# Optimization experiments

Hardware: AMD Instinct MI355X
Metric: run time of the kernel (lower is better)

Reference implementation:

```python
import jax, jax.numpy as jnp
import numpy as np

N_SRC = 2_000_000   # coords at feat_depth (fine level)
N_TGT = 1_000_000   # coords at feat_depth-1 (coarse level)
E = 8_000_000       # neighbor edges from get_neighbours
C = 32              # feature channels


def setup_inputs() -> dict:
    key = jax.random.key(0)
    k1, k2, k3, k4 = jax.random.split(key, 4)
    feat = jax.random.normal(k1, (N_SRC, C), dtype=jnp.float32)
    src_ids = jax.random.randint(k2, (E,), 0, N_SRC)
    tgt_ids = jax.random.randint(k3, (E,), 0, N_TGT)
    ntypes = jax.random.randint(k4, (E, 3), -1, 27).astype(jnp.int32)
    return {"feat": feat, "src_ids": src_ids, "tgt_ids": tgt_ids,
            "ntypes": ntypes, "n_tgt": N_TGT}


def reference(feat, src_ids, tgt_ids, ntypes, n_tgt):
    # p_masks = torch.all(ntypes >= 0, dim=1)
    p_mask = jnp.all(ntypes >= 0, axis=1)                  # [E] bool
    # Route masked-out edges to a dummy segment (index n_tgt) instead of
    # boolean-filtering, keeping shapes static for jit.
    seg = jnp.where(p_mask, tgt_ids, n_tgt)                # [E]
    gathered = feat[src_ids]                               # [E, C] irregular gather
    sums = jax.ops.segment_sum(gathered, seg, num_segments=n_tgt + 1)[:n_tgt]
    counts = jax.ops.segment_sum(jnp.ones((seg.shape[0],), feat.dtype), seg,
                                 num_segments=n_tgt + 1)[:n_tgt]
    # scatter_mean: empty segments yield 0 (torch_scatter semantics)
    out = jnp.where(counts[:, None] > 0, sums / jnp.maximum(counts[:, None], 1), 0.0)
    return out  # feat_depth - 1 is a trivial python int, omitted
```

## Files before the change

### kernel.cpp

```cpp
#include <hip/hip_runtime.h>


#define CCH 32
#define BSH 10
#define BKT 1024
#define CAP 8960
#define BIN_TILE 8192
typedef unsigned int u32;
typedef float f32x4 __attribute__((ext_vector_type(4)));
typedef int i32x4 __attribute__((ext_vector_type(4)));

__global__ __launch_bounds__(1024) void bin_fixed_kernel(
    const int* __restrict__ src_ids, const int* __restrict__ tgt_ids,
    const int* __restrict__ ntypes, u32* __restrict__ bcur,
    u32* __restrict__ pairs, int E, int NB) {
  __shared__ unsigned short s_b[BIN_TILE];
  __shared__ u32 s_pw[BIN_TILE];
  __shared__ u32 s_cnt[1024];
  const long long base = (long long)blockIdx.x * BIN_TILE;

  s_cnt[threadIdx.x] = 0;
  __syncthreads();

  for (int k = 0; k < BIN_TILE / 4096; ++k) {
    const int i4 = (threadIdx.x + k * 1024) * 4;
    const long long e4 = base + i4;
    int n_or[4];
    int tg[4], sr[4];
    bool any = false;
    if (e4 + 3 < E) {
      const i32x4 w0 = __builtin_nontemporal_load(
          reinterpret_cast<const i32x4*>(ntypes + 3 * e4));
      const i32x4 w1 = __builtin_nontemporal_load(
          reinterpret_cast<const i32x4*>(ntypes + 3 * e4 + 4));
      const i32x4 w2 = __builtin_nontemporal_load(
          reinterpret_cast<const i32x4*>(ntypes + 3 * e4 + 8));
      const i32x4 t4 = __builtin_nontemporal_load(
          reinterpret_cast<const i32x4*>(tgt_ids + e4));
      const i32x4 s4 = __builtin_nontemporal_load(
          reinterpret_cast<const i32x4*>(src_ids + e4));
      n_or[0] = w0.x | w0.y | w0.z;
      n_or[1] = w0.w | w1.x | w1.y;
      n_or[2] = w1.z | w1.w | w2.x;
      n_or[3] = w2.y | w2.z | w2.w;
      tg[0] = t4.x; tg[1] = t4.y; tg[2] = t4.z; tg[3] = t4.w;
      sr[0] = s4.x; sr[1] = s4.y; sr[2] = s4.z; sr[3] = s4.w;
      any = true;
    } else {
#pragma unroll
      for (int j = 0; j < 4; ++j) {
        const long long e = e4 + j;
        if (e < E) {
          const long long eb = 3LL * e;
          n_or[j] = ntypes[eb] | ntypes[eb + 1] | ntypes[eb + 2];
          tg[j] = tgt_ids[e];
          sr[j] = src_ids[e];
          any = true;
        } else {
          n_or[j] = -1;
        }
      }
    }
#pragma unroll
    for (int j = 0; j < 4; ++j) {
      unsigned short bb = 0xFFFFu;
      u32 pw = 0;
      if (any && n_or[j] >= 0) {
        const u32 t = (u32)tg[j];
        bb = (unsigned short)(t >> BSH);
        pw = ((u32)sr[j] << BSH) | (t & (BKT - 1u));
        atomicAdd(&s_cnt[bb], 1u);
      }
      s_b[i4 + j] = bb;
      s_pw[i4 + j] = pw;
    }
  }
  __syncthreads();

  if ((int)threadIdx.x < NB) {
    const u32 c = s_cnt[threadIdx.x];
    s_cnt[threadIdx.x] = c ? atomicAdd(&bcur[threadIdx.x], c) : 0u;
  }
  __syncthreads();

  for (int k = 0; k < BIN_TILE / 1024; ++k) {
    const int i = threadIdx.x + k * 1024;
    const unsigned short bb = s_b[i];
    if (bb != 0xFFFFu) {
      const u32 loc = atomicAdd(&s_cnt[bb], 1u);
      if (loc < (u32)CAP) pairs[(u32)bb * (u32)CAP + loc] = s_pw[i];
    }
  }
}

__global__ __launch_bounds__(1024, 8) void sort_gather_kernel(
    const float* __restrict__ feat, const u32* __restrict__ pairs,
    const u32* __restrict__ bcur, float* __restrict__ out, int n_tgt) {
  __shared__ u32 s_pw[CAP];
  __shared__ u32 s_srt[CAP];
  __shared__ u32 s_cnt[BKT];
  __shared__ u32 s_off[BKT];
  __shared__ u32 s_wt[16];
  const int b = blockIdx.x;
  const u32 wbeg = (u32)b * (u32)CAP;
  u32 fill = bcur[b];
  if (fill > (u32)CAP) fill = (u32)CAP;

  for (u32 i = threadIdx.x; i < fill; i += 1024)
    s_pw[i] = __builtin_nontemporal_load(&pairs[wbeg + i]);
  s_cnt[threadIdx.x] = 0;
  __syncthreads();
  for (u32 i = threadIdx.x; i < fill; i += 1024)
    atomicAdd(&s_cnt[s_pw[i] & (BKT - 1u)], 1u);
  __syncthreads();

  const u32 lane = threadIdx.x & 63u;
  const u32 wid = threadIdx.x >> 6;
  const u32 v = s_cnt[threadIdx.x];
  u32 x = v;
#pragma unroll
  for (int d = 1; d < 64; d <<= 1) {
    const u32 y = __shfl_up(x, d, 64);
    if (lane >= (u32)d) x += y;
  }
  if (lane == 63u) s_wt[wid] = x;
  __syncthreads();
  if (wid == 0) {
    u32 w = (lane < 16u) ? s_wt[lane] : 0u;
#pragma unroll
    for (int d = 1; d < 16; d <<= 1) {
      const u32 y = __shfl_up(w, d, 64);
      if (lane >= (u32)d) w += y;
    }
    if (lane < 16u) s_wt[lane] = w;
  }
  __syncthreads();
  const u32 incl = x + (wid ? s_wt[wid - 1] : 0u);
  s_off[threadIdx.x] = incl;
  s_cnt[threadIdx.x] = incl - v;
  __syncthreads();

  for (u32 i = threadIdx.x; i < fill; i += 1024) {
    const u32 pw = s_pw[i];
    const u32 loc = atomicAdd(&s_cnt[pw & (BKT - 1u)], 1u);
    s_srt[loc] = pw >> BSH;
  }
  __syncthreads();

  const int grp = threadIdx.x >> 3;
  const int l4 = (threadIdx.x & 7) * 4;
  const long long t0 = (long long)b << BSH;
  for (int r = grp; r < BKT; r += 128) {
    const long long t = t0 + r;
    if (t >= n_tgt) break;
    const u32 beg = r ? s_off[r - 1] : 0u;
    const u32 n = s_off[r] - beg;
    f32x4 acc = {0.f, 0.f, 0.f, 0.f};
    for (u32 c = 0; c < n; c += 8) {
      const u32 m = n - c;
      u32 idx[8];
#pragma unroll
      for (int k = 0; k < 8; ++k)
        idx[k] = s_srt[beg + c + ((u32)k < m ? (u32)k : 0u)];
      f32x4 vv[8];
#pragma unroll
      for (int k = 0; k < 8; ++k)
        vv[k] = *reinterpret_cast<const f32x4*>(feat +
                                                (long long)idx[k] * CCH + l4);
#pragma unroll
      for (int k = 0; k < 8; ++k) {
        const float w = ((u32)k < m) ? 1.0f : 0.0f;
        acc += vv[k] * w;
      }
    }
    const float inv = n ? 1.0f / (float)n : 0.0f;
    acc *= inv;
    *reinterpret_cast<f32x4*>(out + t * CCH + l4) = acc;
  }
}


__global__ __launch_bounds__(256) void scatter_accum_kernel(
    const float* __restrict__ feat, const int* __restrict__ src_ids,
    const int* __restrict__ tgt_ids, const int* __restrict__ ntypes,
    float* __restrict__ sums, u32* __restrict__ counts,
    long long total_threads) {
  long long tid = (long long)blockIdx.x * blockDim.x + threadIdx.x;
  if (tid >= total_threads) return;
  const int e = (int)(tid >> 3);
  const int g = (int)(tid & 7);
  const long long eb = 3LL * e;
  if ((ntypes[eb] | ntypes[eb + 1] | ntypes[eb + 2]) < 0) return;
  const int s = src_ids[e];
  const int t = tgt_ids[e];
  const float4 v =
      *reinterpret_cast<const float4*>(feat + (long long)s * CCH + g * 4);
  float* dst = sums + (long long)t * CCH + g * 4;
  atomicAdd(dst + 0, v.x);
  atomicAdd(dst + 1, v.y);
  atomicAdd(dst + 2, v.z);
  atomicAdd(dst + 3, v.w);
  if (g == 0) atomicAdd(counts + t, 1u);
}

__global__ __launch_bounds__(256) void finalize_kernel(
    float* __restrict__ out, const u32* __restrict__ counts, int total_vec4) {
  int tid = blockIdx.x * blockDim.x + threadIdx.x;
  if (tid >= total_vec4) return;
  const int t = tid >> 3;
  const u32 cnt = counts[t];
  float4* p = reinterpret_cast<float4*>(out) + tid;
  float4 v = *p;
  const float inv = (cnt > 0u) ? (1.0f / (float)cnt) : 0.0f;
  v.x *= inv; v.y *= inv; v.z *= inv; v.w *= inv;
  *p = v;
}


extern "C" void kernel_launch(void* const* d_in, const int* in_sizes, int n_in,
                              void* d_out, int out_size, void* d_ws,
                              size_t ws_size, hipStream_t stream) {
  const float* feat    = (const float*)d_in[0];
  const int*   src_ids = (const int*)d_in[1];
  const int*   tgt_ids = (const int*)d_in[2];
  const int*   ntypes  = (const int*)d_in[3];
  const int E     = in_sizes[1];
  const int n_src = in_sizes[0] / CCH;
  const int n_tgt = out_size / CCH;

  const int NB = (n_tgt + BKT - 1) >> BSH;

  const size_t need = ((size_t)NB * CAP + NB) * sizeof(u32);
  const long long mean_fill = ((long long)E * BKT + n_tgt - 1) / n_tgt;
  const bool shapes_ok =
      NB <= 1024 && n_src <= (1 << 21) && mean_fill <= 8192;

  if (ws_size >= need && shapes_ok) {
    u32* pairs = (u32*)d_ws;
    u32* bcur  = pairs + (size_t)NB * CAP;

    hipMemsetAsync(bcur, 0, (size_t)NB * sizeof(u32), stream);
    const int bblocks = (E + BIN_TILE - 1) / BIN_TILE;
    bin_fixed_kernel<<<bblocks, 1024, 0, stream>>>(src_ids, tgt_ids, ntypes,
                                                   bcur, pairs, E, NB);
    sort_gather_kernel<<<NB, 1024, 0, stream>>>(feat, pairs, bcur,
                                                (float*)d_out, n_tgt);
  } else {
    float* sums   = (float*)d_out;
    u32*   counts = (u32*)d_ws;
    hipMemsetAsync(d_out, 0, (size_t)out_size * sizeof(float), stream);
    hipMemsetAsync(d_ws, 0, (size_t)n_tgt * sizeof(u32), stream);
    const long long total_threads = (long long)E * 8;
    const long long nblocks = (total_threads + 255) / 256;
    scatter_accum_kernel<<<(dim3)((unsigned int)nblocks), 256, 0, stream>>>(
        feat, src_ids, tgt_ids, ntypes, sums, counts, total_threads);
    const int total_vec4 = n_tgt * 8;
    finalize_kernel<<<(total_vec4 + 255) / 256, 256, 0, stream>>>(
        sums, counts, total_vec4);
  }
}
```

Before: 256.9 us.

## Split gather into two source-half phases to shrink feature working set

The binning key now carries an extra bit saying whether the source index lies in the lower or upper half of feat. The per-block counting sort therefore uses 2048 sub-bins (target row × half). The gather first accumulates all rows from lower-half sources, then from upper-half sources, keeping 8 per-row accumulators in registers. The aim is to halve the feature working set touched by concurrently running blocks, so more gather reads hit cache. In exchange, register pressure and scan work go up, the gather batch drops from 8 to 4 loads, and CAP shrinks to make room for the larger shared-memory histograms, which lowers overflow headroom per bucket.

```diff
diff --git a/kernel.cpp b/kernel.cpp
--- a/kernel.cpp
+++ b/kernel.cpp
@@ -4,7 +4,7 @@
 #define CCH 32
 #define BSH 10
 #define BKT 1024
-#define CAP 8960
+#define CAP 8064
 #define BIN_TILE 8192
 typedef unsigned int u32;
 typedef float f32x4 __attribute__((ext_vector_type(4)));
@@ -13,7 +13,7 @@
 __global__ __launch_bounds__(1024) void bin_fixed_kernel(
     const int* __restrict__ src_ids, const int* __restrict__ tgt_ids,
     const int* __restrict__ ntypes, u32* __restrict__ bcur,
-    u32* __restrict__ pairs, int E, int NB) {
+    u32* __restrict__ pairs, int E, int NB, int half_src) {
   __shared__ unsigned short s_b[BIN_TILE];
   __shared__ u32 s_pw[BIN_TILE];
   __shared__ u32 s_cnt[1024];
@@ -68,7 +68,8 @@
       if (any && n_or[j] >= 0) {
         const u32 t = (u32)tg[j];
         bb = (unsigned short)(t >> BSH);
-        pw = ((u32)sr[j] << BSH) | (t & (BKT - 1u));
+        pw = ((u32)sr[j] << 11) | ((t & (BKT - 1u)) << 1) |
+             (u32)(sr[j] >= half_src);
         atomicAdd(&s_cnt[bb], 1u);
       }
       s_b[i4 + j] = bb;
@@ -98,8 +99,8 @@
     const u32* __restrict__ bcur, float* __restrict__ out, int n_tgt) {
   __shared__ u32 s_pw[CAP];
   __shared__ u32 s_srt[CAP];
-  __shared__ u32 s_cnt[BKT];
-  __shared__ u32 s_off[BKT];
+  __shared__ u32 s_cnt[2048];
+  __shared__ u32 s_off[2048];
   __shared__ u32 s_wt[16];
   const int b = blockIdx.x;
   const u32 wbeg = (u32)b * (u32)CAP;
@@ -109,15 +110,17 @@
   for (u32 i = threadIdx.x; i < fill; i += 1024)
     s_pw[i] = __builtin_nontemporal_load(&pairs[wbeg + i]);
   s_cnt[threadIdx.x] = 0;
+  s_cnt[threadIdx.x + 1024] = 0;
   __syncthreads();
   for (u32 i = threadIdx.x; i < fill; i += 1024)
-    atomicAdd(&s_cnt[s_pw[i] & (BKT - 1u)], 1u);
+    atomicAdd(&s_cnt[s_pw[i] & 2047u], 1u);
   __syncthreads();
 
   const u32 lane = threadIdx.x & 63u;
   const u32 wid = threadIdx.x >> 6;
-  const u32 v = s_cnt[threadIdx.x];
-  u32 x = v;
+  const u32 i2 = threadIdx.x * 2;
+  const u32 v0 = s_cnt[i2], v1 = s_cnt[i2 + 1];
+  u32 x = v0 + v1;
 #pragma unroll
   for (int d = 1; d < 64; d <<= 1) {
     const u32 y = __shfl_up(x, d, 64);
@@ -136,46 +139,66 @@
   }
   __syncthreads();
   const u32 incl = x + (wid ? s_wt[wid - 1] : 0u);
-  s_off[threadIdx.x] = incl;
-  s_cnt[threadIdx.x] = incl - v;
+  s_off[i2] = incl - v1;
+  s_off[i2 + 1] = incl;
+  s_cnt[i2] = incl - v1 - v0;
+  s_cnt[i2 + 1] = incl - v1;
   __syncthreads();
 
   for (u32 i = threadIdx.x; i < fill; i += 1024) {
     const u32 pw = s_pw[i];
-    const u32 loc = atomicAdd(&s_cnt[pw & (BKT - 1u)], 1u);
-    s_srt[loc] = pw >> BSH;
+    const u32 loc = atomicAdd(&s_cnt[pw & 2047u], 1u);
+    s_srt[loc] = pw >> 11;
   }
   __syncthreads();
 
   const int grp = threadIdx.x >> 3;
   const int l4 = (threadIdx.x & 7) * 4;
   const long long t0 = (long long)b << BSH;
-  for (int r = grp; r < BKT; r += 128) {
+
+  f32x4 acc[8];
+#pragma unroll
+  for (int rr = 0; rr < 8; ++rr) acc[rr] = (f32x4){0.f, 0.f, 0.f, 0.f};
+
+#pragma unroll
+  for (int phase = 0; phase < 2; ++phase) {
+#pragma unroll
+    for (int rr = 0; rr < 8; ++rr) {
+      const int r = grp + rr * 128;
+      const int bin = (r << 1) | phase;
+      const u32 beg = bin ? s_off[bin - 1] : 0u;
+      const u32 n = s_off[bin] - beg;
+      for (u32 c = 0; c < n; c += 4) {
+        const u32 m = n - c;
+        u32 idx[4];
+#pragma unroll
+        for (int k = 0; k < 4; ++k)
+          idx[k] = s_srt[beg + c + ((u32)k < m ? (u32)k : 0u)];
+        f32x4 vv[4];
+#pragma unroll
+        for (int k = 0; k < 4; ++k)
+          vv[k] = *reinterpret_cast<const f32x4*>(
+              feat + (long long)idx[k] * CCH + l4);
+#pragma unroll
+        for (int k = 0; k < 4; ++k) {
+          const float w = ((u32)k < m) ? 1.0f : 0.0f;
+          acc[rr] += vv[k] * w;
+        }
+      }
+    }
+  }
+
+#pragma unroll
+  for (int rr = 0; rr < 8; ++rr) {
+    const int r = grp + rr * 128;
     const long long t = t0 + r;
-    if (t >= n_tgt) break;
-    const u32 beg = r ? s_off[r - 1] : 0u;
-    const u32 n = s_off[r] - beg;
-    f32x4 acc = {0.f, 0.f, 0.f, 0.f};
-    for (u32 c = 0; c < n; c += 8) {
-      const u32 m = n - c;
-      u32 idx[8];
-#pragma unroll
-      for (int k = 0; k < 8; ++k)
-        idx[k] = s_srt[beg + c + ((u32)k < m ? (u32)k : 0u)];
-      f32x4 vv[8];
-#pragma unroll
-      for (int k = 0; k < 8; ++k)
-        vv[k] = *reinterpret_cast<const f32x4*>(feat +
-                                                (long long)idx[k] * CCH + l4);
-#pragma unroll
-      for (int k = 0; k < 8; ++k) {
-        const float w = ((u32)k < m) ? 1.0f : 0.0f;
-        acc += vv[k] * w;
-      }
-    }
-    const float inv = n ? 1.0f / (float)n : 0.0f;
-    acc *= inv;
-    *reinterpret_cast<f32x4*>(out + t * CCH + l4) = acc;
+    if (t < n_tgt) {
+      const u32 bA = (u32)(r << 1);
+      const u32 beg = bA ? s_off[bA - 1] : 0u;
+      const u32 n = s_off[bA + 1] - beg;
+      const float inv = n ? 1.0f / (float)n : 0.0f;
+      *reinterpret_cast<f32x4*>(out + t * CCH + l4) = acc[rr] * inv;
+    }
   }
 }
 
@@ -241,8 +264,8 @@
 
     hipMemsetAsync(bcur, 0, (size_t)NB * sizeof(u32), stream);
     const int bblocks = (E + BIN_TILE - 1) / BIN_TILE;
-    bin_fixed_kernel<<<bblocks, 1024, 0, stream>>>(src_ids, tgt_ids, ntypes,
-                                                   bcur, pairs, E, NB);
+    bin_fixed_kernel<<<bblocks, 1024, 0, stream>>>(
+        src_ids, tgt_ids, ntypes, bcur, pairs, E, NB, n_src >> 1);
     sort_gather_kernel<<<NB, 1024, 0, stream>>>(feat, pairs, bcur,
                                                 (float*)d_out, n_tgt);
   } else {
```

New measurement: 258.5 us. No clear change (+0.6%).

## Convert features to bf16 alongside binning and gather bf16 in sort kernel

Applied to the files above, without the earlier changes.

Adds a combined kernel where even blocks convert the fp32 feature table to bf16 in workspace while odd blocks do the edge binning. The sort-gather kernel then gathers 8-byte bf16 rows instead of 16-byte fp32 rows and widens them back to fp32 for accumulation, with a nontemporal output store. This roughly halves the random gather traffic, at the cost of an extra full pass over feat and reduced input precision, which may exceed the tolerance. The previous fp32 path stays as a fallback when workspace is too small.

```diff
diff --git a/kernel.cpp b/kernel.cpp
--- a/kernel.cpp
+++ b/kernel.cpp
@@ -7,17 +7,45 @@
 #define CAP 8960
 #define BIN_TILE 8192
 typedef unsigned int u32;
+typedef unsigned short u16;
 typedef float f32x4 __attribute__((ext_vector_type(4)));
 typedef int i32x4 __attribute__((ext_vector_type(4)));
-
-__global__ __launch_bounds__(1024) void bin_fixed_kernel(
-    const int* __restrict__ src_ids, const int* __restrict__ tgt_ids,
-    const int* __restrict__ ntypes, u32* __restrict__ bcur,
-    u32* __restrict__ pairs, int E, int NB) {
+typedef unsigned short u16x4 __attribute__((ext_vector_type(4)));
+
+
+__global__ __launch_bounds__(1024) void convert_bin_kernel(
+    const float* __restrict__ feat, const int* __restrict__ src_ids,
+    const int* __restrict__ tgt_ids, const int* __restrict__ ntypes,
+    u32* __restrict__ bcur, u32* __restrict__ pairs, u16* __restrict__ bf,
+    int E, int NB, long long n_vec4) {
   __shared__ unsigned short s_b[BIN_TILE];
   __shared__ u32 s_pw[BIN_TILE];
   __shared__ u32 s_cnt[1024];
-  const long long base = (long long)blockIdx.x * BIN_TILE;
+
+  const int half = (int)(gridDim.x >> 1);
+  if ((blockIdx.x & 1u) == 0u) {
+    const int cb = (int)(blockIdx.x >> 1);
+    const long long stride = (long long)half * 1024;
+    for (long long i = (long long)cb * 1024 + threadIdx.x; i < n_vec4;
+         i += stride) {
+      const f32x4 v = __builtin_nontemporal_load(
+          reinterpret_cast<const f32x4*>(feat) + i);
+      const u32 b0 = __float_as_uint(v.x);
+      const u32 b1 = __float_as_uint(v.y);
+      const u32 b2 = __float_as_uint(v.z);
+      const u32 b3 = __float_as_uint(v.w);
+      u16x4 o;
+      o.x = (u16)((b0 + 0x7FFFu + ((b0 >> 16) & 1u)) >> 16);
+      o.y = (u16)((b1 + 0x7FFFu + ((b1 >> 16) & 1u)) >> 16);
+      o.z = (u16)((b2 + 0x7FFFu + ((b2 >> 16) & 1u)) >> 16);
+      o.w = (u16)((b3 + 0x7FFFu + ((b3 >> 16) & 1u)) >> 16);
+      reinterpret_cast<u16x4*>(bf)[i] = o;
+    }
+    return;
+  }
+
+  const int bb = (int)(blockIdx.x >> 1);
+  const long long base = (long long)bb * BIN_TILE;
 
   s_cnt[threadIdx.x] = 0;
   __syncthreads();
@@ -63,15 +91,15 @@
     }
 #pragma unroll
     for (int j = 0; j < 4; ++j) {
-      unsigned short bb = 0xFFFFu;
+      unsigned short bbid = 0xFFFFu;
       u32 pw = 0;
       if (any && n_or[j] >= 0) {
         const u32 t = (u32)tg[j];
-        bb = (unsigned short)(t >> BSH);
+        bbid = (unsigned short)(t >> BSH);
         pw = ((u32)sr[j] << BSH) | (t & (BKT - 1u));
-        atomicAdd(&s_cnt[bb], 1u);
-      }
-      s_b[i4 + j] = bb;
+        atomicAdd(&s_cnt[bbid], 1u);
+      }
+      s_b[i4 + j] = bbid;
       s_pw[i4 + j] = pw;
     }
   }
@@ -85,10 +113,183 @@
 
   for (int k = 0; k < BIN_TILE / 1024; ++k) {
     const int i = threadIdx.x + k * 1024;
-    const unsigned short bb = s_b[i];
-    if (bb != 0xFFFFu) {
-      const u32 loc = atomicAdd(&s_cnt[bb], 1u);
-      if (loc < (u32)CAP) pairs[(u32)bb * (u32)CAP + loc] = s_pw[i];
+    const unsigned short bbid = s_b[i];
+    if (bbid != 0xFFFFu) {
+      const u32 loc = atomicAdd(&s_cnt[bbid], 1u);
+      if (loc < (u32)CAP) pairs[(u32)bbid * (u32)CAP + loc] = s_pw[i];
+    }
+  }
+}
+
+__global__ __launch_bounds__(1024, 8) void sort_gather_bf16_kernel(
+    const u16* __restrict__ bf, const u32* __restrict__ pairs,
+    const u32* __restrict__ bcur, float* __restrict__ out, int n_tgt) {
+  __shared__ u32 s_pw[CAP];
+  __shared__ u32 s_srt[CAP];
+  __shared__ u32 s_cnt[BKT];
+  __shared__ u32 s_off[BKT];
+  __shared__ u32 s_wt[16];
+  const int b = blockIdx.x;
+  const u32 wbeg = (u32)b * (u32)CAP;
+  u32 fill = bcur[b];
+  if (fill > (u32)CAP) fill = (u32)CAP;
+
+  for (u32 i = threadIdx.x; i < fill; i += 1024)
+    s_pw[i] = __builtin_nontemporal_load(&pairs[wbeg + i]);
+  s_cnt[threadIdx.x] = 0;
+  __syncthreads();
+  for (u32 i = threadIdx.x; i < fill; i += 1024)
+    atomicAdd(&s_cnt[s_pw[i] & (BKT - 1u)], 1u);
+  __syncthreads();
+
+  const u32 lane = threadIdx.x & 63u;
+  const u32 wid = threadIdx.x >> 6;
+  const u32 v = s_cnt[threadIdx.x];
+  u32 x = v;
+#pragma unroll
+  for (int d = 1; d < 64; d <<= 1) {
+    const u32 y = __shfl_up(x, d, 64);
+    if (lane >= (u32)d) x += y;
+  }
+  if (lane == 63u) s_wt[wid] = x;
+  __syncthreads();
+  if (wid == 0) {
+    u32 w = (lane < 16u) ? s_wt[lane] : 0u;
+#pragma unroll
+    for (int d = 1; d < 16; d <<= 1) {
+      const u32 y = __shfl_up(w, d, 64);
+      if (lane >= (u32)d) w += y;
+    }
+    if (lane < 16u) s_wt[lane] = w;
+  }
+  __syncthreads();
+  const u32 incl = x + (wid ? s_wt[wid - 1] : 0u);
+  s_off[threadIdx.x] = incl;
+  s_cnt[threadIdx.x] = incl - v;
+  __syncthreads();
+
+  for (u32 i = threadIdx.x; i < fill; i += 1024) {
+    const u32 pw = s_pw[i];
+    const u32 loc = atomicAdd(&s_cnt[pw & (BKT - 1u)], 1u);
+    s_srt[loc] = pw >> BSH;
+  }
+  __syncthreads();
+
+  const int grp = threadIdx.x >> 3;
+  const int g = threadIdx.x & 7;
+  const long long t0 = (long long)b << BSH;
+  const u16x4* bfv = reinterpret_cast<const u16x4*>(bf);
+  for (int r = grp; r < BKT; r += 128) {
+    const long long t = t0 + r;
+    if (t >= n_tgt) break;
+    const u32 beg = r ? s_off[r - 1] : 0u;
+    const u32 n = s_off[r] - beg;
+    f32x4 acc = {0.f, 0.f, 0.f, 0.f};
+    for (u32 c = 0; c < n; c += 8) {
+      const u32 m = n - c;
+      u32 idx[8];
+#pragma unroll
+      for (int k = 0; k < 8; ++k)
+        idx[k] = s_srt[beg + c + ((u32)k < m ? (u32)k : 0u)];
+      u16x4 hv[8];
+#pragma unroll
+      for (int k = 0; k < 8; ++k)
+        hv[k] = bfv[(long long)idx[k] * 8 + g];
+#pragma unroll
+      for (int k = 0; k < 8; ++k) {
+        const float w = ((u32)k < m) ? 1.0f : 0.0f;
+        f32x4 f;
+        f.x = __uint_as_float((u32)hv[k].x << 16);
+        f.y = __uint_as_float((u32)hv[k].y << 16);
+        f.z = __uint_as_float((u32)hv[k].z << 16);
+        f.w = __uint_as_float((u32)hv[k].w << 16);
+        acc += f * w;
+      }
+    }
+    const float inv = n ? 1.0f / (float)n : 0.0f;
+    acc *= inv;
+    __builtin_nontemporal_store(
+        acc, reinterpret_cast<f32x4*>(out + t * CCH + g * 4));
+  }
+}
+
+
+__global__ __launch_bounds__(1024) void bin_fixed_kernel(
+    const int* __restrict__ src_ids, const int* __restrict__ tgt_ids,
+    const int* __restrict__ ntypes, u32* __restrict__ bcur,
+    u32* __restrict__ pairs, int E, int NB) {
+  __shared__ unsigned short s_b[BIN_TILE];
+  __shared__ u32 s_pw[BIN_TILE];
+  __shared__ u32 s_cnt[1024];
+  const long long base = (long long)blockIdx.x * BIN_TILE;
+
+  s_cnt[threadIdx.x] = 0;
+  __syncthreads();
+  for (int k = 0; k < BIN_TILE / 4096; ++k) {
+    const int i4 = (threadIdx.x + k * 1024) * 4;
+    const long long e4 = base + i4;
+    int n_or[4];
+    int tg[4], sr[4];
+    bool any = false;
+    if (e4 + 3 < E) {
+      const i32x4 w0 = __builtin_nontemporal_load(
+          reinterpret_cast<const i32x4*>(ntypes + 3 * e4));
+      const i32x4 w1 = __builtin_nontemporal_load(
+          reinterpret_cast<const i32x4*>(ntypes + 3 * e4 + 4));
+      const i32x4 w2 = __builtin_nontemporal_load(
+          reinterpret_cast<const i32x4*>(ntypes + 3 * e4 + 8));
+      const i32x4 t4 = __builtin_nontemporal_load(
+          reinterpret_cast<const i32x4*>(tgt_ids + e4));
+      const i32x4 s4 = __builtin_nontemporal_load(
+          reinterpret_cast<const i32x4*>(src_ids + e4));
+      n_or[0] = w0.x | w0.y | w0.z;
+      n_or[1] = w0.w | w1.x | w1.y;
+      n_or[2] = w1.z | w1.w | w2.x;
+      n_or[3] = w2.y | w2.z | w2.w;
+      tg[0] = t4.x; tg[1] = t4.y; tg[2] = t4.z; tg[3] = t4.w;
+      sr[0] = s4.x; sr[1] = s4.y; sr[2] = s4.z; sr[3] = s4.w;
+      any = true;
+    } else {
+#pragma unroll
+      for (int j = 0; j < 4; ++j) {
+        const long long e = e4 + j;
+        if (e < E) {
+          const long long eb = 3LL * e;
+          n_or[j] = ntypes[eb] | ntypes[eb + 1] | ntypes[eb + 2];
+          tg[j] = tgt_ids[e];
+          sr[j] = src_ids[e];
+          any = true;
+        } else {
+          n_or[j] = -1;
+        }
+      }
+    }
+#pragma unroll
+    for (int j = 0; j < 4; ++j) {
+      unsigned short bbid = 0xFFFFu;
+      u32 pw = 0;
+      if (any && n_or[j] >= 0) {
+        const u32 t = (u32)tg[j];
+        bbid = (unsigned short)(t >> BSH);
+        pw = ((u32)sr[j] << BSH) | (t & (BKT - 1u));
+        atomicAdd(&s_cnt[bbid], 1u);
+      }
+      s_b[i4 + j] = bbid;
+      s_pw[i4 + j] = pw;
+    }
+  }
+  __syncthreads();
+  if ((int)threadIdx.x < NB) {
+    const u32 c = s_cnt[threadIdx.x];
+    s_cnt[threadIdx.x] = c ? atomicAdd(&bcur[threadIdx.x], c) : 0u;
+  }
+  __syncthreads();
+  for (int k = 0; k < BIN_TILE / 1024; ++k) {
+    const int i = threadIdx.x + k * 1024;
+    const unsigned short bbid = s_b[i];
+    if (bbid != 0xFFFFu) {
+      const u32 loc = atomicAdd(&s_cnt[bbid], 1u);
+      if (loc < (u32)CAP) pairs[(u32)bbid * (u32)CAP + loc] = s_pw[i];
     }
   }
 }
@@ -229,18 +430,33 @@
   const int n_tgt = out_size / CCH;
 
   const int NB = (n_tgt + BKT - 1) >> BSH;
-
-  const size_t need = ((size_t)NB * CAP + NB) * sizeof(u32);
+  const int bblocks = (E + BIN_TILE - 1) / BIN_TILE;
+
+  const size_t pairs_u32 = (size_t)NB * CAP;
+  const size_t base_u32 = (pairs_u32 + (size_t)NB + 3) & ~(size_t)3;
+  const size_t need_f32 = (pairs_u32 + (size_t)NB) * sizeof(u32);
+  const size_t need_bf16 =
+      base_u32 * sizeof(u32) + (size_t)n_src * CCH * sizeof(u16);
   const long long mean_fill = ((long long)E * BKT + n_tgt - 1) / n_tgt;
   const bool shapes_ok =
       NB <= 1024 && n_src <= (1 << 21) && mean_fill <= 8192;
 
-  if (ws_size >= need && shapes_ok) {
+  if (ws_size >= need_bf16 && shapes_ok) {
     u32* pairs = (u32*)d_ws;
-    u32* bcur  = pairs + (size_t)NB * CAP;
+    u32* bcur  = pairs + pairs_u32;
+    u16* bf    = (u16*)((u32*)d_ws + base_u32);
 
     hipMemsetAsync(bcur, 0, (size_t)NB * sizeof(u32), stream);
-    const int bblocks = (E + BIN_TILE - 1) / BIN_TILE;
+    const long long n_vec4 = (long long)n_src * 8;
+    convert_bin_kernel<<<2 * bblocks, 1024, 0, stream>>>(
+        feat, src_ids, tgt_ids, ntypes, bcur, pairs, bf, E, NB, n_vec4);
+    sort_gather_bf16_kernel<<<NB, 1024, 0, stream>>>(bf, pairs, bcur,
+                                                     (float*)d_out, n_tgt);
+  } else if (ws_size >= need_f32 && shapes_ok) {
+    u32* pairs = (u32*)d_ws;
+    u32* bcur  = pairs + pairs_u32;
+
+    hipMemsetAsync(bcur, 0, (size_t)NB * sizeof(u32), stream);
     bin_fixed_kernel<<<bblocks, 1024, 0, stream>>>(src_ids, tgt_ids, ntypes,
                                                    bcur, pairs, E, NB);
     sort_gather_kernel<<<NB, 1024, 0, stream>>>(feat, pairs, bcur,
```

Result: slower. 356.8 us (+38.9%).
